# Kernel optimization log

Hardware: AMD Instinct MI355X
Metric: run time of the kernel (lower is better)

The kernel has to match this reference:

```python
import jax, jax.numpy as jnp
import numpy as np


def _closest_dist_sum(p1, p2):
    # p1: [B, N, 3], p2: [B, M, 3]
    # Euclidean distance via the expanded quadratic form; matches
    # torch.norm(p1 - p2, 2, dim=3) -> min over p2 -> sum over all.
    d2 = (jnp.sum(p1 * p1, axis=-1)[:, :, None]
          + jnp.sum(p2 * p2, axis=-1)[:, None, :]
          - 2.0 * jnp.einsum('bnd,bmd->bnm', p1, p2))  # [B, N, M]
    d = jnp.sqrt(jnp.maximum(d2, 0.0))
    return jnp.sum(jnp.min(d, axis=2))


def setup_inputs() -> dict:
    key = jax.random.key(0)
    k1, k2 = jax.random.split(key)
    shape_xyz = jax.random.normal(k1, (8, 8192, 6), dtype=jnp.float32)
    skel_xyz = jax.random.normal(k2, (8, 2048, 3), dtype=jnp.float32)
    return {"shape_xyz": shape_xyz, "skel_xyz": skel_xyz}


def reference(shape_xyz, skel_xyz):
    # normals (shape_xyz[:, :, 3:6]) are extracted but unused in the loss
    pts = shape_xyz[:, :, :3]
    cd1 = _closest_dist_sum(pts, skel_xyz)   # shape -> skeleton
    cd2 = _closest_dist_sum(skel_xyz, pts)   # skeleton -> shape
    loss_cd = (cd1 + cd2) * 0.0001
    return loss_cd
```

## Files before the change

kernel.cpp:

```cpp
#include <hip/hip_runtime.h>

#define BATCH   8
#define SHAPE_N 8192
#define SKEL_M  2048
#define CHUNK   512

#define WS2_OFF 512
#define SKC_OFF 66048
#define SHC_OFF (66048 + 131072)

typedef short bf16x8 __attribute__((ext_vector_type(8)));
typedef float f32x16 __attribute__((ext_vector_type(16)));
union FragU { bf16x8 v; uint4 u4; };

__device__ __forceinline__ unsigned int f2bf(float a) {
    unsigned int u = __float_as_uint(a);
    return (u + 0x7FFFu + ((u >> 16) & 1u)) >> 16;
}
__device__ __forceinline__ float bf2f(unsigned int h) {
    return __uint_as_float(h << 16);
}
__device__ __forceinline__ unsigned int pack2(unsigned int lo, unsigned int hi) {
    return lo | (hi << 16);
}
__device__ __forceinline__ void bfsplit(float v, unsigned int& h, unsigned int& l) {
    h = f2bf(v);
    l = f2bf(v - bf2f(h));
}

__device__ __forceinline__ void conv_point(float bx, float by, float bz,
                                           uint4& hi, uint4& lo) {
    const float cx = -2.f * bx, cy = -2.f * by, cz = -2.f * bz;
    const float rb = bx * bx + by * by + bz * bz;
    unsigned int chx, clx, chy, cly, chz, clz, rbh, rbl;
    bfsplit(cx, chx, clx); bfsplit(cy, chy, cly); bfsplit(cz, chz, clz);
    bfsplit(rb, rbh, rbl);
    hi = make_uint4(pack2(chx, chy), pack2(chz, rbh),
                    pack2(chx, chy), pack2(chz, rbl));
    lo = make_uint4(pack2(clx, cly), pack2(clz, 0u), 0u, 0u);
}

__device__ __forceinline__ void gl16(const char* g, char* l) {
    __builtin_amdgcn_global_load_lds(
        (const __attribute__((address_space(1))) void*)g,
        (__attribute__((address_space(3))) void*)l, 16, 0, 0);
}

__global__ __launch_bounds__(256) void cd_prep(
    const float* __restrict__ shape, const float* __restrict__ skel,
    float* __restrict__ ws)
{
    const int p = blockIdx.x * 256 + threadIdx.x;
    const float* q;
    uint4* dst;
    int idx;
    if (p < BATCH * SKEL_M) {
        const int b = p >> 11; idx = p & (SKEL_M - 1);
        q = skel + (size_t)p * 3;
        dst = (uint4*)(ws + SKC_OFF) + (size_t)b * 4096;
    } else {
        const int s = p - BATCH * SKEL_M;
        const int b = s >> 13; idx = s & (SHAPE_N - 1);
        q = shape + (size_t)s * 6;
        dst = (uint4*)(ws + SHC_OFF) + (size_t)b * 16384;
    }
    uint4 hi, lo;
    conv_point(q[0], q[1], q[2], hi, lo);
    const int g = idx >> 5, r = idx & 31;
    dst[g * 64 + r]      = hi;
    dst[g * 64 + 32 + r] = lo;
}

template <int SA>
__device__ __forceinline__ void cd_scan2(
    const float* __restrict__ Araw,
    const uint4* __restrict__ Bconv,
    uint4* __restrict__ sB,
    float* rmin, float* ra)
{
    const int tid = threadIdx.x;
    const int l = tid & 63, wv = tid >> 6;
    const unsigned int one = 0x3F80u;

    FragU bf[4];
#pragma unroll
    for (int j = 0; j < 4; ++j) {
        const float* p = Araw + (size_t)(j * 32 + (l & 31)) * SA;
        const float x = p[0], y = p[1], z = p[2];
        ra[j] = x * x + y * y + z * z;
        unsigned int hx, lx, hy, ly, hz, lz;
        bfsplit(x, hx, lx); bfsplit(y, hy, ly); bfsplit(z, hz, lz);
        if (l < 32)
            bf[j].u4 = make_uint4(pack2(hx, hy), pack2(hz, one),
                                  pack2(lx, ly), pack2(lz, one));
        else
            bf[j].u4 = make_uint4(pack2(hx, hy), pack2(hz, 0u), 0u, 0u);
        rmin[j] = 3.4e38f;
    }

    const f32x16 Z = {0,0,0,0,0,0,0,0,0,0,0,0,0,0,0,0};
    const char* gbase = (const char*)Bconv;
    char* lbase = (char*)sB;

#pragma unroll
    for (int k = 0; k < 4; ++k)
        gl16(gbase + k * 4096 + tid * 16, lbase + k * 4096 + tid * 16);
    __syncthreads();

    for (int c = 0; c < 4; ++c) {
        if (c < 3) {
            const char* src = gbase + (c + 1) * 16384;
            char* dstl = lbase + (((c + 1) & 1) ? 16384 : 0);
#pragma unroll
            for (int k = 0; k < 4; ++k)
                gl16(src + k * 4096 + tid * 16, dstl + k * 4096 + tid * 16);
        }
        unsigned int o = (unsigned int)(((c & 1) ? 16384 : 0) + wv * 4096 +
                                        (l >> 5) * 512 + (l & 31) * 16);
#pragma unroll
        for (int g = 0; g < 4; ++g) {
            FragU af;
            af.u4 = *(const uint4*)(lbase + o);
            o += 1024;
#pragma unroll
            for (int j = 0; j < 4; ++j) {
                f32x16 D = __builtin_amdgcn_mfma_f32_32x32x16_bf16(
                    af.v, bf[j].v, Z, 0, 0, 0);
                const float t0 = fminf(fminf(D[0],  D[1]),  D[2]);
                const float t1 = fminf(fminf(D[3],  D[4]),  D[5]);
                const float t2 = fminf(fminf(D[6],  D[7]),  D[8]);
                const float t3 = fminf(fminf(D[9],  D[10]), D[11]);
                const float t4 = fminf(fminf(D[12], D[13]), D[14]);
                const float u0 = fminf(fminf(t0, t1), t2);
                const float u1 = fminf(fminf(t3, t4), D[15]);
                rmin[j] = fminf(rmin[j], fminf(u0, u1));
            }
        }
        __syncthreads();
    }
#pragma unroll
    for (int j = 0; j < 4; ++j)
        rmin[j] = fminf(rmin[j], __shfl_xor(rmin[j], 32, 64));
}

__global__ __launch_bounds__(256, 4) void cd_main(
    const float* __restrict__ shape, const float* __restrict__ skel,
    float* __restrict__ ws)
{
    __shared__ uint4 sB[CHUNK * 4];
    __shared__ float smin[4][128];
    __shared__ float sra[128];
    __shared__ float s_wsum[2];
    const int tid = threadIdx.x;
    const int l = tid & 63, wv = tid >> 6;
    const int bid = blockIdx.x;
    float rmin[4], ra[4];

    if (bid < 512) {
        const int b = bid >> 6, sub = bid & 63;
        cd_scan2<6>(shape + ((size_t)b * SHAPE_N + sub * 128) * 6,
                    (const uint4*)(ws + SKC_OFF) + (size_t)b * 4096,
                    sB, rmin, ra);
    } else {
        const int j = bid - 512;
        const int b = j >> 6, rem = j & 63;
        const int asub = rem >> 2, bs = rem & 3;
        cd_scan2<3>(skel + ((size_t)b * SKEL_M + asub * 128) * 3,
                    (const uint4*)(ws + SHC_OFF) + (size_t)b * 16384 + bs * 4096,
                    sB, rmin, ra);
    }

    if (l < 32) {
#pragma unroll
        for (int j = 0; j < 4; ++j) smin[wv][j * 32 + l] = rmin[j];
        if (wv == 0) {
#pragma unroll
            for (int j = 0; j < 4; ++j) sra[j * 32 + l] = ra[j];
        }
    }
    __syncthreads();

    if (bid < 512) {
        float d = 0.f;
        if (tid < 128) {
            const float m = fminf(fminf(smin[0][tid], smin[1][tid]),
                                  fminf(smin[2][tid], smin[3][tid]));
            d = sqrtf(fmaxf(sra[tid] + m, 0.f));
        }
        for (int o = 32; o; o >>= 1) d += __shfl_down(d, o, 64);
        if (l == 0 && wv < 2) s_wsum[wv] = d;
        __syncthreads();
        if (tid == 0) ws[bid] = s_wsum[0] + s_wsum[1];
    } else {
        if (tid < 128) {
            const int j = bid - 512;
            const int b = j >> 6, rem = j & 63;
            const int asub = rem >> 2, bs = rem & 3;
            const float m = fminf(fminf(smin[0][tid], smin[1][tid]),
                                  fminf(smin[2][tid], smin[3][tid]));
            ws[WS2_OFF + bs * (BATCH * SKEL_M) + b * SKEL_M +
               asub * 128 + tid] = sra[tid] + m;
        }
    }
}

__global__ __launch_bounds__(1024) void cd_reduce(
    const float* __restrict__ ws, float* __restrict__ out)
{
    __shared__ float s_wsum[16];
    const int t = threadIdx.x;
    float s = 0.f;

    const float4* w4 = (const float4*)(ws + WS2_OFF);
#pragma unroll
    for (int r = 0; r < 4; ++r) {
        const int i4 = r * 1024 + t;
        float4 v0 = w4[i4];
        const float4 v1 = w4[4096 + i4];
        const float4 v2 = w4[8192 + i4];
        const float4 v3 = w4[12288 + i4];
        v0.x = fminf(fminf(v0.x, v1.x), fminf(v2.x, v3.x));
        v0.y = fminf(fminf(v0.y, v1.y), fminf(v2.y, v3.y));
        v0.z = fminf(fminf(v0.z, v1.z), fminf(v2.z, v3.z));
        v0.w = fminf(fminf(v0.w, v1.w), fminf(v2.w, v3.w));
        s += sqrtf(fmaxf(v0.x, 0.f)) + sqrtf(fmaxf(v0.y, 0.f)) +
             sqrtf(fmaxf(v0.z, 0.f)) + sqrtf(fmaxf(v0.w, 0.f));
    }
    if (t < 512) s += ws[t];

    for (int o = 32; o; o >>= 1) s += __shfl_down(s, o, 64);
    const int lane = t & 63, wave = t >> 6;
    if (lane == 0) s_wsum[wave] = s;
    __syncthreads();
    if (t == 0) {
        float tot = 0.f;
#pragma unroll
        for (int w = 0; w < 16; ++w) tot += s_wsum[w];
        out[0] = tot * 1e-4f;
    }
}

extern "C" void kernel_launch(void* const* d_in, const int* in_sizes, int n_in,
                              void* d_out, int out_size, void* d_ws, size_t ws_size,
                              hipStream_t stream) {
    const float* shape = (const float*)d_in[0];
    const float* skel  = (const float*)d_in[1];
    float* out         = (float*)d_out;
    float* ws          = (float*)d_ws;

    cd_prep<<<320, 256, 0, stream>>>(shape, skel, ws);
    cd_main<<<1024, 256, 0, stream>>>(shape, skel, ws);
    cd_reduce<<<1, 1024, 0, stream>>>(ws, out);
}
```

Baseline: 73.60 us.

## Fuse final reduction into main kernel via last-block atomic counter

Skeleton-to-shape blocks now each cover 32 skeleton points against the full shape cloud (16 chunks). That lets every block finish its own min and sqrt and emit a single partial sum, instead of writing per-slice minima for a separate kernel to merge. The separate reduce kernel is removed. A global atomic counter, reset in the prep kernel, lets the last block to finish sum the 1024 partials and write the output. This saves one kernel launch and the workspace round trip, at the cost of longer per-block loops with 4x fewer MFMAs per LDS fragment load for the skeleton side.

```diff
diff --git a/kernel.cpp b/kernel.cpp
--- a/kernel.cpp
+++ b/kernel.cpp
@@ -5,9 +5,9 @@
 #define SKEL_M  2048
 #define CHUNK   512
 
-#define WS2_OFF 512
-#define SKC_OFF 66048
-#define SHC_OFF (66048 + 131072)
+#define CNT_OFF 1024
+#define SKC_OFF 2048
+#define SHC_OFF (2048 + 131072)
 
 typedef short bf16x8 __attribute__((ext_vector_type(8)));
 typedef float f32x16 __attribute__((ext_vector_type(16)));
@@ -50,6 +50,9 @@
     const float* __restrict__ shape, const float* __restrict__ skel,
     float* __restrict__ ws)
 {
+    if (blockIdx.x == 0 && threadIdx.x == 0)
+        ((int*)ws)[CNT_OFF] = 0;
+
     const int p = blockIdx.x * 256 + threadIdx.x;
     const float* q;
     uint4* dst;
@@ -71,8 +74,8 @@
     dst[g * 64 + 32 + r] = lo;
 }
 
-template <int SA>
-__device__ __forceinline__ void cd_scan2(
+template <int NFRAG, int NCHUNK, int SA>
+__device__ __forceinline__ void cd_scan(
     const float* __restrict__ Araw,
     const uint4* __restrict__ Bconv,
     uint4* __restrict__ sB,
@@ -82,9 +85,9 @@
     const int l = tid & 63, wv = tid >> 6;
     const unsigned int one = 0x3F80u;
 
-    FragU bf[4];
-#pragma unroll
-    for (int j = 0; j < 4; ++j) {
+    FragU bf[NFRAG];
+#pragma unroll
+    for (int j = 0; j < NFRAG; ++j) {
         const float* p = Araw + (size_t)(j * 32 + (l & 31)) * SA;
         const float x = p[0], y = p[1], z = p[2];
         ra[j] = x * x + y * y + z * z;
@@ -107,9 +110,9 @@
         gl16(gbase + k * 4096 + tid * 16, lbase + k * 4096 + tid * 16);
     __syncthreads();
 
-    for (int c = 0; c < 4; ++c) {
-        if (c < 3) {
-            const char* src = gbase + (c + 1) * 16384;
+    for (int c = 0; c < NCHUNK; ++c) {
+        if (c + 1 < NCHUNK) {
+            const char* src = gbase + (size_t)(c + 1) * 16384;
             char* dstl = lbase + (((c + 1) & 1) ? 16384 : 0);
 #pragma unroll
             for (int k = 0; k < 4; ++k)
@@ -123,7 +126,7 @@
             af.u4 = *(const uint4*)(lbase + o);
             o += 1024;
 #pragma unroll
-            for (int j = 0; j < 4; ++j) {
+            for (int j = 0; j < NFRAG; ++j) {
                 f32x16 D = __builtin_amdgcn_mfma_f32_32x32x16_bf16(
                     af.v, bf[j].v, Z, 0, 0, 0);
                 const float t0 = fminf(fminf(D[0],  D[1]),  D[2]);
@@ -139,48 +142,39 @@
         __syncthreads();
     }
 #pragma unroll
-    for (int j = 0; j < 4; ++j)
+    for (int j = 0; j < NFRAG; ++j)
         rmin[j] = fminf(rmin[j], __shfl_xor(rmin[j], 32, 64));
 }
 
 __global__ __launch_bounds__(256, 4) void cd_main(
     const float* __restrict__ shape, const float* __restrict__ skel,
-    float* __restrict__ ws)
+    float* __restrict__ ws, float* __restrict__ out)
 {
     __shared__ uint4 sB[CHUNK * 4];
     __shared__ float smin[4][128];
     __shared__ float sra[128];
-    __shared__ float s_wsum[2];
+    __shared__ float s_wsum[4];
+    __shared__ int s_last;
     const int tid = threadIdx.x;
     const int l = tid & 63, wv = tid >> 6;
     const int bid = blockIdx.x;
     float rmin[4], ra[4];
+    float blocksum = 0.f;
 
     if (bid < 512) {
         const int b = bid >> 6, sub = bid & 63;
-        cd_scan2<6>(shape + ((size_t)b * SHAPE_N + sub * 128) * 6,
-                    (const uint4*)(ws + SKC_OFF) + (size_t)b * 4096,
-                    sB, rmin, ra);
-    } else {
-        const int j = bid - 512;
-        const int b = j >> 6, rem = j & 63;
-        const int asub = rem >> 2, bs = rem & 3;
-        cd_scan2<3>(skel + ((size_t)b * SKEL_M + asub * 128) * 3,
-                    (const uint4*)(ws + SHC_OFF) + (size_t)b * 16384 + bs * 4096,
-                    sB, rmin, ra);
-    }
-
-    if (l < 32) {
-#pragma unroll
-        for (int j = 0; j < 4; ++j) smin[wv][j * 32 + l] = rmin[j];
-        if (wv == 0) {
-#pragma unroll
-            for (int j = 0; j < 4; ++j) sra[j * 32 + l] = ra[j];
-        }
-    }
-    __syncthreads();
-
-    if (bid < 512) {
+        cd_scan<4, 4, 6>(shape + ((size_t)b * SHAPE_N + sub * 128) * 6,
+                         (const uint4*)(ws + SKC_OFF) + (size_t)b * 4096,
+                         sB, rmin, ra);
+        if (l < 32) {
+#pragma unroll
+            for (int j = 0; j < 4; ++j) smin[wv][j * 32 + l] = rmin[j];
+            if (wv == 0) {
+#pragma unroll
+                for (int j = 0; j < 4; ++j) sra[j * 32 + l] = ra[j];
+            }
+        }
+        __syncthreads();
         float d = 0.f;
         if (tid < 128) {
             const float m = fminf(fminf(smin[0][tid], smin[1][tid]),
@@ -188,55 +182,46 @@
             d = sqrtf(fmaxf(sra[tid] + m, 0.f));
         }
         for (int o = 32; o; o >>= 1) d += __shfl_down(d, o, 64);
-        if (l == 0 && wv < 2) s_wsum[wv] = d;
-        __syncthreads();
-        if (tid == 0) ws[bid] = s_wsum[0] + s_wsum[1];
+        if (l == 0) s_wsum[wv] = d;
+        __syncthreads();
+        if (tid == 0)
+            blocksum = s_wsum[0] + s_wsum[1] + s_wsum[2] + s_wsum[3];
     } else {
-        if (tid < 128) {
-            const int j = bid - 512;
-            const int b = j >> 6, rem = j & 63;
-            const int asub = rem >> 2, bs = rem & 3;
+        const int j = bid - 512;
+        const int b = j >> 6, sub = j & 63;
+        cd_scan<1, 16, 3>(skel + ((size_t)b * SKEL_M + sub * 32) * 3,
+                          (const uint4*)(ws + SHC_OFF) + (size_t)b * 16384,
+                          sB, rmin, ra);
+        if (l < 32) {
+            smin[wv][l] = rmin[0];
+            if (wv == 0) sra[l] = ra[0];
+        }
+        __syncthreads();
+        float d = 0.f;
+        if (tid < 32) {
             const float m = fminf(fminf(smin[0][tid], smin[1][tid]),
                                   fminf(smin[2][tid], smin[3][tid]));
-            ws[WS2_OFF + bs * (BATCH * SKEL_M) + b * SKEL_M +
-               asub * 128 + tid] = sra[tid] + m;
-        }
-    }
-}
-
-__global__ __launch_bounds__(1024) void cd_reduce(
-    const float* __restrict__ ws, float* __restrict__ out)
-{
-    __shared__ float s_wsum[16];
-    const int t = threadIdx.x;
-    float s = 0.f;
-
-    const float4* w4 = (const float4*)(ws + WS2_OFF);
-#pragma unroll
-    for (int r = 0; r < 4; ++r) {
-        const int i4 = r * 1024 + t;
-        float4 v0 = w4[i4];
-        const float4 v1 = w4[4096 + i4];
-        const float4 v2 = w4[8192 + i4];
-        const float4 v3 = w4[12288 + i4];
-        v0.x = fminf(fminf(v0.x, v1.x), fminf(v2.x, v3.x));
-        v0.y = fminf(fminf(v0.y, v1.y), fminf(v2.y, v3.y));
-        v0.z = fminf(fminf(v0.z, v1.z), fminf(v2.z, v3.z));
-        v0.w = fminf(fminf(v0.w, v1.w), fminf(v2.w, v3.w));
-        s += sqrtf(fmaxf(v0.x, 0.f)) + sqrtf(fmaxf(v0.y, 0.f)) +
-             sqrtf(fmaxf(v0.z, 0.f)) + sqrtf(fmaxf(v0.w, 0.f));
-    }
-    if (t < 512) s += ws[t];
-
-    for (int o = 32; o; o >>= 1) s += __shfl_down(s, o, 64);
-    const int lane = t & 63, wave = t >> 6;
-    if (lane == 0) s_wsum[wave] = s;
+            d = sqrtf(fmaxf(sra[tid] + m, 0.f));
+        }
+        for (int o = 32; o; o >>= 1) d += __shfl_down(d, o, 64);
+        if (tid == 0) blocksum = d;
+    }
+
+    if (tid == 0) {
+        ws[bid] = blocksum;
+        __threadfence();
+        const int old = atomicAdd((int*)ws + CNT_OFF, 1);
+        s_last = (old == 1023);
+    }
     __syncthreads();
-    if (t == 0) {
-        float tot = 0.f;
-#pragma unroll
-        for (int w = 0; w < 16; ++w) tot += s_wsum[w];
-        out[0] = tot * 1e-4f;
+    if (s_last) {
+        __threadfence();
+        float s = ws[tid] + ws[tid + 256] + ws[tid + 512] + ws[tid + 768];
+        for (int o = 32; o; o >>= 1) s += __shfl_down(s, o, 64);
+        if (l == 0) s_wsum[wv] = s;
+        __syncthreads();
+        if (tid == 0)
+            out[0] = (s_wsum[0] + s_wsum[1] + s_wsum[2] + s_wsum[3]) * 1e-4f;
     }
 }
 
@@ -249,6 +234,5 @@
     float* ws          = (float*)d_ws;
 
     cd_prep<<<320, 256, 0, stream>>>(shape, skel, ws);
-    cd_main<<<1024, 256, 0, stream>>>(shape, skel, ws);
-    cd_reduce<<<1, 1024, 0, stream>>>(ws, out);
-}
+    cd_main<<<1024, 256, 0, stream>>>(shape, skel, ws, out);
+}
```

New measurement: 94.79 us. 1.29x slower.

## Fuse final reduction via last-block atomic and read B fragments directly from global

Applied to the files above, without the earlier changes.

Removes the separate single-block reduce kernel by having the last block of the main kernel (detected with an atomic counter reset in the prep kernel) perform the final min/sqrt/sum reduction. Also drops the LDS double-buffered staging of the converted point fragments and loads them straight from global memory in the MFMA loop, eliminating block barriers and shared memory. This trades a kernel launch and LDS traffic for an atomic, thread fences, and reliance on L2/L1 caching of the fragment reads. The tail reduction now runs on only 256 threads instead of 1024.

```diff
diff --git a/kernel.cpp b/kernel.cpp
--- a/kernel.cpp
+++ b/kernel.cpp
@@ -3,11 +3,11 @@
 #define BATCH   8
 #define SHAPE_N 8192
 #define SKEL_M  2048
-#define CHUNK   512
 
 #define WS2_OFF 512
-#define SKC_OFF 66048
-#define SHC_OFF (66048 + 131072)
+#define CNT_OFF 66048
+#define SKC_OFF 66176
+#define SHC_OFF (66176 + 131072)
 
 typedef short bf16x8 __attribute__((ext_vector_type(8)));
 typedef float f32x16 __attribute__((ext_vector_type(16)));
@@ -40,16 +40,13 @@
     lo = make_uint4(pack2(clx, cly), pack2(clz, 0u), 0u, 0u);
 }
 
-__device__ __forceinline__ void gl16(const char* g, char* l) {
-    __builtin_amdgcn_global_load_lds(
-        (const __attribute__((address_space(1))) void*)g,
-        (__attribute__((address_space(3))) void*)l, 16, 0, 0);
-}
-
 __global__ __launch_bounds__(256) void cd_prep(
     const float* __restrict__ shape, const float* __restrict__ skel,
     float* __restrict__ ws)
 {
+    if (blockIdx.x == 0 && threadIdx.x == 0)
+        ((int*)ws)[CNT_OFF] = 0;
+
     const int p = blockIdx.x * 256 + threadIdx.x;
     const float* q;
     uint4* dst;
@@ -75,7 +72,6 @@
 __device__ __forceinline__ void cd_scan2(
     const float* __restrict__ Araw,
     const uint4* __restrict__ Bconv,
-    uint4* __restrict__ sB,
     float* rmin, float* ra)
 {
     const int tid = threadIdx.x;
@@ -99,44 +95,26 @@
     }
 
     const f32x16 Z = {0,0,0,0,0,0,0,0,0,0,0,0,0,0,0,0};
-    const char* gbase = (const char*)Bconv;
-    char* lbase = (char*)sB;
-
-#pragma unroll
-    for (int k = 0; k < 4; ++k)
-        gl16(gbase + k * 4096 + tid * 16, lbase + k * 4096 + tid * 16);
-    __syncthreads();
-
-    for (int c = 0; c < 4; ++c) {
-        if (c < 3) {
-            const char* src = gbase + (c + 1) * 16384;
-            char* dstl = lbase + (((c + 1) & 1) ? 16384 : 0);
-#pragma unroll
-            for (int k = 0; k < 4; ++k)
-                gl16(src + k * 4096 + tid * 16, dstl + k * 4096 + tid * 16);
-        }
-        unsigned int o = (unsigned int)(((c & 1) ? 16384 : 0) + wv * 4096 +
-                                        (l >> 5) * 512 + (l & 31) * 16);
-#pragma unroll
-        for (int g = 0; g < 4; ++g) {
-            FragU af;
-            af.u4 = *(const uint4*)(lbase + o);
-            o += 1024;
-#pragma unroll
-            for (int j = 0; j < 4; ++j) {
-                f32x16 D = __builtin_amdgcn_mfma_f32_32x32x16_bf16(
-                    af.v, bf[j].v, Z, 0, 0, 0);
-                const float t0 = fminf(fminf(D[0],  D[1]),  D[2]);
-                const float t1 = fminf(fminf(D[3],  D[4]),  D[5]);
-                const float t2 = fminf(fminf(D[6],  D[7]),  D[8]);
-                const float t3 = fminf(fminf(D[9],  D[10]), D[11]);
-                const float t4 = fminf(fminf(D[12], D[13]), D[14]);
-                const float u0 = fminf(fminf(t0, t1), t2);
-                const float u1 = fminf(fminf(t3, t4), D[15]);
-                rmin[j] = fminf(rmin[j], fminf(u0, u1));
-            }
-        }
-        __syncthreads();
+    const char* p0 = (const char*)Bconv + wv * 16384 +
+                     (l >> 5) * 512 + (l & 31) * 16;
+
+#pragma unroll 8
+    for (int g = 0; g < 16; ++g) {
+        FragU af;
+        af.u4 = *(const uint4*)(p0 + g * 1024);
+#pragma unroll
+        for (int j = 0; j < 4; ++j) {
+            f32x16 D = __builtin_amdgcn_mfma_f32_32x32x16_bf16(
+                af.v, bf[j].v, Z, 0, 0, 0);
+            const float t0 = fminf(fminf(D[0],  D[1]),  D[2]);
+            const float t1 = fminf(fminf(D[3],  D[4]),  D[5]);
+            const float t2 = fminf(fminf(D[6],  D[7]),  D[8]);
+            const float t3 = fminf(fminf(D[9],  D[10]), D[11]);
+            const float t4 = fminf(fminf(D[12], D[13]), D[14]);
+            const float u0 = fminf(fminf(t0, t1), t2);
+            const float u1 = fminf(fminf(t3, t4), D[15]);
+            rmin[j] = fminf(rmin[j], fminf(u0, u1));
+        }
     }
 #pragma unroll
     for (int j = 0; j < 4; ++j)
@@ -145,12 +123,12 @@
 
 __global__ __launch_bounds__(256, 4) void cd_main(
     const float* __restrict__ shape, const float* __restrict__ skel,
-    float* __restrict__ ws)
+    float* __restrict__ ws, float* __restrict__ out)
 {
-    __shared__ uint4 sB[CHUNK * 4];
     __shared__ float smin[4][128];
     __shared__ float sra[128];
-    __shared__ float s_wsum[2];
+    __shared__ float s_wsum[4];
+    __shared__ int s_last;
     const int tid = threadIdx.x;
     const int l = tid & 63, wv = tid >> 6;
     const int bid = blockIdx.x;
@@ -160,14 +138,14 @@
         const int b = bid >> 6, sub = bid & 63;
         cd_scan2<6>(shape + ((size_t)b * SHAPE_N + sub * 128) * 6,
                     (const uint4*)(ws + SKC_OFF) + (size_t)b * 4096,
-                    sB, rmin, ra);
+                    rmin, ra);
     } else {
         const int j = bid - 512;
         const int b = j >> 6, rem = j & 63;
         const int asub = rem >> 2, bs = rem & 3;
         cd_scan2<3>(skel + ((size_t)b * SKEL_M + asub * 128) * 3,
                     (const uint4*)(ws + SHC_OFF) + (size_t)b * 16384 + bs * 4096,
-                    sB, rmin, ra);
+                    rmin, ra);
     }
 
     if (l < 32) {
@@ -202,41 +180,38 @@
                asub * 128 + tid] = sra[tid] + m;
         }
     }
-}
-
-__global__ __launch_bounds__(1024) void cd_reduce(
-    const float* __restrict__ ws, float* __restrict__ out)
-{
-    __shared__ float s_wsum[16];
-    const int t = threadIdx.x;
-    float s = 0.f;
-
-    const float4* w4 = (const float4*)(ws + WS2_OFF);
-#pragma unroll
-    for (int r = 0; r < 4; ++r) {
-        const int i4 = r * 1024 + t;
-        float4 v0 = w4[i4];
-        const float4 v1 = w4[4096 + i4];
-        const float4 v2 = w4[8192 + i4];
-        const float4 v3 = w4[12288 + i4];
-        v0.x = fminf(fminf(v0.x, v1.x), fminf(v2.x, v3.x));
-        v0.y = fminf(fminf(v0.y, v1.y), fminf(v2.y, v3.y));
-        v0.z = fminf(fminf(v0.z, v1.z), fminf(v2.z, v3.z));
-        v0.w = fminf(fminf(v0.w, v1.w), fminf(v2.w, v3.w));
-        s += sqrtf(fmaxf(v0.x, 0.f)) + sqrtf(fmaxf(v0.y, 0.f)) +
-             sqrtf(fmaxf(v0.z, 0.f)) + sqrtf(fmaxf(v0.w, 0.f));
-    }
-    if (t < 512) s += ws[t];
-
-    for (int o = 32; o; o >>= 1) s += __shfl_down(s, o, 64);
-    const int lane = t & 63, wave = t >> 6;
-    if (lane == 0) s_wsum[wave] = s;
+
+    __threadfence();
     __syncthreads();
-    if (t == 0) {
-        float tot = 0.f;
-#pragma unroll
-        for (int w = 0; w < 16; ++w) tot += s_wsum[w];
-        out[0] = tot * 1e-4f;
+    if (tid == 0) {
+        const int old = atomicAdd((int*)ws + CNT_OFF, 1);
+        s_last = (old == 1023);
+    }
+    __syncthreads();
+    if (s_last) {
+        __threadfence();
+        float s = 0.f;
+        const float4* w4 = (const float4*)(ws + WS2_OFF);
+#pragma unroll
+        for (int r = 0; r < 16; ++r) {
+            const int i4 = r * 256 + tid;
+            float4 v0 = w4[i4];
+            const float4 v1 = w4[4096 + i4];
+            const float4 v2 = w4[8192 + i4];
+            const float4 v3 = w4[12288 + i4];
+            v0.x = fminf(fminf(v0.x, v1.x), fminf(v2.x, v3.x));
+            v0.y = fminf(fminf(v0.y, v1.y), fminf(v2.y, v3.y));
+            v0.z = fminf(fminf(v0.z, v1.z), fminf(v2.z, v3.z));
+            v0.w = fminf(fminf(v0.w, v1.w), fminf(v2.w, v3.w));
+            s += sqrtf(fmaxf(v0.x, 0.f)) + sqrtf(fmaxf(v0.y, 0.f)) +
+                 sqrtf(fmaxf(v0.z, 0.f)) + sqrtf(fmaxf(v0.w, 0.f));
+        }
+        s += ws[tid] + ws[tid + 256];
+        for (int o = 32; o; o >>= 1) s += __shfl_down(s, o, 64);
+        if (l == 0) s_wsum[wv] = s;
+        __syncthreads();
+        if (tid == 0)
+            out[0] = (s_wsum[0] + s_wsum[1] + s_wsum[2] + s_wsum[3]) * 1e-4f;
     }
 }
 
@@ -249,6 +224,5 @@
     float* ws          = (float*)d_ws;
 
     cd_prep<<<320, 256, 0, stream>>>(shape, skel, ws);
-    cd_main<<<1024, 256, 0, stream>>>(shape, skel, ws);
-    cd_reduce<<<1, 1024, 0, stream>>>(ws, out);
-}
+    cd_main<<<1024, 256, 0, stream>>>(shape, skel, ws, out);
+}
```

Result: slower. 138.1 us (+87.6%).
